# Performance work log

Measured on AMD Instinct MI355X. Metric: run time of the kernel, lower is better.

Reference implementation:

```python
import jax, jax.numpy as jnp
import numpy as np

D = 128
SCALE = 1.0 / np.sqrt(D)  # scalar_value


def setup_inputs() -> dict:
    key = jax.random.key(0)
    k1, k2, k3 = jax.random.split(key, 3)
    B, N, S = 2, 16, 2048
    q = jax.random.normal(k1, (B, N, S, D), dtype=jnp.float32)
    k = jax.random.normal(k2, (B, N, S, D), dtype=jnp.float32)
    v = jax.random.normal(k3, (B, N, S, D), dtype=jnp.float32)
    return {"q": q, "k": k, "v": v}


def reference(q, k, v):
    # BNSD layout. scores = scale * Q K^T, causal mask, softmax with
    # explicit max/sum tracking (golden for NPU fusion attention).
    s1, s2 = q.shape[2], k.shape[2]
    scores = jnp.einsum('bnsd,bntd->bnst', q, k) * SCALE
    # generate_attn_mask: causal (lower-triangular kept), masked -> -inf
    causal = jnp.triu(jnp.ones((s1, s2), dtype=bool), k=1)
    scores = jnp.where(causal, -jnp.inf, scores)
    softmax_max = jnp.max(scores, axis=-1, keepdims=True)          # [B,N,S,1]
    exp_scores = jnp.exp(scores - softmax_max)
    softmax_sum = jnp.sum(exp_scores, axis=-1, keepdims=True)      # [B,N,S,1]
    softmax_res = exp_scores / softmax_sum
    out = jnp.einsum('bnst,bntd->bnsd', softmax_res, v)
    # NPU golden repeats stats x8 along last dim
    return (out,
            jnp.tile(softmax_max, (1, 1, 1, 8)),
            jnp.tile(softmax_sum, (1, 1, 1, 8)))
```

## Files before the change

### kernel.cpp

```cpp
#include <hip/hip_runtime.h>
#include <math.h>
#include <stdint.h>

#define D_DIM 128
#define SEQ 2048
#define NHEADS 32
#define BC 64
#define SCALE 0.08838834764831843f

typedef short bf16x8 __attribute__((ext_vector_type(8)));
typedef float f32x4 __attribute__((ext_vector_type(4)));

union Frag { uint32_t u[4]; bf16x8 v; unsigned short s[8]; };
union Pack8 { unsigned short s[8]; uint4 q; };

__device__ __forceinline__ uint32_t fbits(float x) { return __builtin_bit_cast(uint32_t, x); }
__device__ __forceinline__ float bbits(uint32_t u) { return __builtin_bit_cast(float, u); }
__device__ __forceinline__ unsigned short bf16_rne(float x) {
    uint32_t u = fbits(x);
    u += 0x7FFFu + ((u >> 16) & 1u);
    return (unsigned short)(u >> 16);
}
__device__ __forceinline__ void split2(float a, float b, uint32_t& hp, uint32_t& lp) {
    uint32_t ua = fbits(a) & 0xFFFF0000u, ub = fbits(b) & 0xFFFF0000u;
    float la = a - bbits(ua), lb = b - bbits(ub);
    hp = (ua >> 16) | ub;
    lp = (fbits(la) >> 16) | (fbits(lb) & 0xFFFF0000u);
}

__global__ __launch_bounds__(512, 2) void fa_fused(
    const float* __restrict__ q, const float* __restrict__ k,
    const float* __restrict__ v, float* __restrict__ out)
{
    __shared__ __align__(16) unsigned short Khs[64 * 128];
    __shared__ __align__(16) unsigned short Kls[64 * 128];
    __shared__ __align__(16) unsigned short Vhs[128 * 64];
    __shared__ __align__(16) unsigned short Pbs[128 * 64];

    const int x = blockIdx.x;
    const int it = 15 - (x >> 5);
    const int h = x & 31;

    const int t    = (int)threadIdx.x;
    const int wb   = t >> 6;
    const int lane = t & 63;
    const int ln   = lane & 15;
    const int qd   = lane >> 4;

    const float* qh = q + (size_t)h * SEQ * D_DIM;
    const float* kh = k + (size_t)h * SEQ * D_DIM;
    const float* vh = v + (size_t)h * SEQ * D_DIM;
    float* out_o = out;
    float* out_m = out + (size_t)NHEADS * SEQ * D_DIM;
    float* out_l = out_m + (size_t)NHEADS * SEQ * 8;

    const int qrow0 = it * 128 + wb * 16;

    const int krow0 = t >> 5;
    const int kd4   = t & 31;

    Frag Qh[4], Ql[4];
    {
        const float* qp = qh + (size_t)(qrow0 + ln) * D_DIM;
        #pragma unroll
        for (int kc = 0; kc < 4; ++kc) {
            const int kb = kc * 32 + qd * 8;
            float e[8];
            *(float4*)(e)     = *(const float4*)(qp + kb);
            *(float4*)(e + 4) = *(const float4*)(qp + kb + 4);
            #pragma unroll
            for (int j = 0; j < 8; ++j) e[j] *= SCALE;
            #pragma unroll
            for (int j = 0; j < 4; ++j)
                split2(e[2 * j], e[2 * j + 1], Qh[kc].u[j], Ql[kc].u[j]);
        }
    }

    float4 kreg[4];
    #pragma unroll
    for (int itr = 0; itr < 4; ++itr)
        kreg[itr] = *(const float4*)(kh + (size_t)(itr * 16 + krow0) * D_DIM + kd4 * 4);

    f32x4 accO[8];
    float m_r[4], l_r[4];
    #pragma unroll
    for (int nd = 0; nd < 8; ++nd) accO[nd] = (f32x4){0.f, 0.f, 0.f, 0.f};
    #pragma unroll
    for (int r = 0; r < 4; ++r) { m_r[r] = -INFINITY; l_r[r] = 0.f; }

    const int jt_end = 2 * it + 1;
    for (int jt = 0; jt <= jt_end; ++jt) {
        const int c0 = jt * BC;

        __syncthreads();

        float vreg[2][8];
        #pragma unroll
        for (int uu = 0; uu < 2; ++uu) {
            const int ug = wb * 2 + uu;
            const int cc = ug >> 1;
            const int d  = (ug & 1) * 64 + lane;
            #pragma unroll
            for (int j = 0; j < 8; ++j)
                vreg[uu][j] = vh[(size_t)(c0 + cc * 8 + j) * D_DIM + d];
        }
        #pragma unroll
        for (int itr = 0; itr < 4; ++itr) {
            const int row = itr * 16 + krow0;
            uint32_t hp0, lp0, hp1, lp1;
            split2(kreg[itr].x, kreg[itr].y, hp0, lp0);
            split2(kreg[itr].z, kreg[itr].w, hp1, lp1);
            const int off = row * 128 + (((kd4 >> 1) ^ (row & 7)) * 8) + (kd4 & 1) * 4;
            *(uint2*)(Khs + off) = make_uint2(hp0, hp1);
            *(uint2*)(Kls + off) = make_uint2(lp0, lp1);
        }
        #pragma unroll
        for (int uu = 0; uu < 2; ++uu) {
            const int ug = wb * 2 + uu;
            const int cc = ug >> 1;
            const int d  = (ug & 1) * 64 + lane;
            Pack8 p8;
            #pragma unroll
            for (int j = 0; j < 8; ++j) p8.s[j] = bf16_rne(vreg[uu][j]);
            *(uint4*)(Vhs + d * 64 + ((cc ^ (d & 7)) * 8)) = p8.q;
        }

        __syncthreads();

        if (jt < jt_end) {
            const float* kp2 = kh + (size_t)(c0 + BC) * D_DIM;
            #pragma unroll
            for (int itr = 0; itr < 4; ++itr)
                kreg[itr] = *(const float4*)(kp2 + (size_t)(itr * 16 + krow0) * D_DIM + kd4 * 4);
        }

        if (c0 <= qrow0 + 15) {
            f32x4 accS[4];
            #pragma unroll
            for (int nt = 0; nt < 4; ++nt) accS[nt] = (f32x4){0.f, 0.f, 0.f, 0.f};
            #pragma unroll
            for (int kc = 0; kc < 4; ++kc) {
                #pragma unroll
                for (int nt = 0; nt < 4; ++nt) {
                    int n = nt * 16 + ln;
                    int off = n * 128 + (((kc * 4 + qd) ^ (n & 7)) * 8);
                    Frag Bh, Bl;
                    Bh.v = *(const bf16x8*)(Khs + off);
                    Bl.v = *(const bf16x8*)(Kls + off);
                    f32x4 c = accS[nt];
                    c = __builtin_amdgcn_mfma_f32_16x16x32_bf16(Qh[kc].v, Bh.v, c, 0, 0, 0);
                    c = __builtin_amdgcn_mfma_f32_16x16x32_bf16(Qh[kc].v, Bl.v, c, 0, 0, 0);
                    c = __builtin_amdgcn_mfma_f32_16x16x32_bf16(Ql[kc].v, Bh.v, c, 0, 0, 0);
                    accS[nt] = c;
                }
            }
            const bool needMask = (c0 + 63 > qrow0);
            #pragma unroll
            for (int r = 0; r < 4; ++r) {
                const int rowg = qrow0 + qd * 4 + r;
                float sv[4], mx = -INFINITY;
                #pragma unroll
                for (int nt = 0; nt < 4; ++nt) {
                    float s = accS[nt][r];
                    if (needMask && (c0 + nt * 16 + ln > rowg)) s = -INFINITY;
                    sv[nt] = s; mx = fmaxf(mx, s);
                }
                #pragma unroll
                for (int off = 1; off < 16; off <<= 1) mx = fmaxf(mx, __shfl_xor(mx, off));
                const float mnew = fmaxf(m_r[r], mx);
                const float alpha = __expf(m_r[r] - mnew);
                float p[4];
                #pragma unroll
                for (int nt = 0; nt < 4; ++nt) p[nt] = __expf(sv[nt] - mnew);
                m_r[r] = mnew;
                l_r[r] = l_r[r] * alpha + ((p[0] + p[1]) + (p[2] + p[3]));
                #pragma unroll
                for (int nd = 0; nd < 8; ++nd) accO[nd][r] *= alpha;
                const int R = wb * 16 + qd * 4 + r;
                #pragma unroll
                for (int nt = 0; nt < 4; ++nt) {
                    int c = nt * 16 + ln;
                    Pbs[R * 64 + (((c >> 3) ^ (R & 7)) * 8) + (c & 7)] = bf16_rne(p[nt]);
                }
            }
            #pragma unroll
            for (int kc2 = 0; kc2 < 2; ++kc2) {
                Frag Pf;
                const int R = wb * 16 + ln;
                Pf.v = *(const bf16x8*)(Pbs + R * 64 + (((kc2 * 4 + qd) ^ (R & 7)) * 8));
                #pragma unroll
                for (int nd = 0; nd < 8; ++nd) {
                    int dcol = nd * 16 + ln;
                    int voff = dcol * 64 + (((kc2 * 4 + qd) ^ (dcol & 7)) * 8);
                    Frag Vh2;
                    Vh2.v = *(const bf16x8*)(Vhs + voff);
                    accO[nd] = __builtin_amdgcn_mfma_f32_16x16x32_bf16(Pf.v, Vh2.v, accO[nd], 0, 0, 0);
                }
            }
        }
    }

    #pragma unroll
    for (int r = 0; r < 4; ++r) {
        #pragma unroll
        for (int off = 1; off < 16; off <<= 1) l_r[r] += __shfl_xor(l_r[r], off);
    }
    #pragma unroll
    for (int r = 0; r < 4; ++r) {
        const int rowg = qrow0 + qd * 4 + r;
        const float invl = 1.0f / l_r[r];
        float* op = out_o + (size_t)h * SEQ * D_DIM + (size_t)rowg * D_DIM;
        #pragma unroll
        for (int nd = 0; nd < 8; ++nd) op[nd * 16 + ln] = accO[nd][r] * invl;
        if (ln < 8) {
            size_t sb = ((size_t)h * SEQ + rowg) * 8 + ln;
            out_m[sb] = m_r[r];
            out_l[sb] = l_r[r];
        }
    }
}

extern "C" void kernel_launch(void* const* d_in, const int* in_sizes, int n_in,
                              void* d_out, int out_size, void* d_ws, size_t ws_size,
                              hipStream_t stream) {
    const float* q = (const float*)d_in[0];
    const float* k = (const float*)d_in[1];
    const float* v = (const float*)d_in[2];
    float* out = (float*)d_out;
    (void)d_ws; (void)ws_size;

    fa_fused<<<dim3(512), dim3(512), 0, stream>>>(q, k, v, out);
}
```

Before: 244.6 us.

## Prefetch V tiles into registers and skip rescale when row max unchanged

```diff
diff --git a/kernel.cpp b/kernel.cpp
--- a/kernel.cpp
+++ b/kernel.cpp
@@ -58,6 +58,8 @@
 
     const int krow0 = t >> 5;
     const int kd4   = t & 31;
+    const int vcc   = wb;
+    const int vd0   = lane;
 
     Frag Qh[4], Ql[4];
     {
@@ -77,9 +79,35 @@
     }
 
     float4 kreg[4];
+    float  vraw[2][8];
+    uint2  khi[4], klo[4];
+    uint4  vcv[2];
+
     #pragma unroll
     for (int itr = 0; itr < 4; ++itr)
         kreg[itr] = *(const float4*)(kh + (size_t)(itr * 16 + krow0) * D_DIM + kd4 * 4);
+    #pragma unroll
+    for (int uu = 0; uu < 2; ++uu) {
+        const int d = uu * 64 + vd0;
+        #pragma unroll
+        for (int j = 0; j < 8; ++j)
+            vraw[uu][j] = vh[(size_t)(vcc * 8 + j) * D_DIM + d];
+    }
+    #pragma unroll
+    for (int itr = 0; itr < 4; ++itr) {
+        uint32_t hp0, lp0, hp1, lp1;
+        split2(kreg[itr].x, kreg[itr].y, hp0, lp0);
+        split2(kreg[itr].z, kreg[itr].w, hp1, lp1);
+        khi[itr] = make_uint2(hp0, hp1);
+        klo[itr] = make_uint2(lp0, lp1);
+    }
+    #pragma unroll
+    for (int uu = 0; uu < 2; ++uu) {
+        Pack8 p8;
+        #pragma unroll
+        for (int j = 0; j < 8; ++j) p8.s[j] = bf16_rne(vraw[uu][j]);
+        vcv[uu] = p8.q;
+    }
 
     f32x4 accO[8];
     float m_r[4], l_r[4];
@@ -94,44 +122,34 @@
 
         __syncthreads();
 
-        float vreg[2][8];
-        #pragma unroll
-        for (int uu = 0; uu < 2; ++uu) {
-            const int ug = wb * 2 + uu;
-            const int cc = ug >> 1;
-            const int d  = (ug & 1) * 64 + lane;
-            #pragma unroll
-            for (int j = 0; j < 8; ++j)
-                vreg[uu][j] = vh[(size_t)(c0 + cc * 8 + j) * D_DIM + d];
-        }
         #pragma unroll
         for (int itr = 0; itr < 4; ++itr) {
             const int row = itr * 16 + krow0;
-            uint32_t hp0, lp0, hp1, lp1;
-            split2(kreg[itr].x, kreg[itr].y, hp0, lp0);
-            split2(kreg[itr].z, kreg[itr].w, hp1, lp1);
             const int off = row * 128 + (((kd4 >> 1) ^ (row & 7)) * 8) + (kd4 & 1) * 4;
-            *(uint2*)(Khs + off) = make_uint2(hp0, hp1);
-            *(uint2*)(Kls + off) = make_uint2(lp0, lp1);
+            *(uint2*)(Khs + off) = khi[itr];
+            *(uint2*)(Kls + off) = klo[itr];
         }
         #pragma unroll
         for (int uu = 0; uu < 2; ++uu) {
-            const int ug = wb * 2 + uu;
-            const int cc = ug >> 1;
-            const int d  = (ug & 1) * 64 + lane;
-            Pack8 p8;
-            #pragma unroll
-            for (int j = 0; j < 8; ++j) p8.s[j] = bf16_rne(vreg[uu][j]);
-            *(uint4*)(Vhs + d * 64 + ((cc ^ (d & 7)) * 8)) = p8.q;
+            const int d = uu * 64 + vd0;
+            *(uint4*)(Vhs + d * 64 + ((vcc ^ (d & 7)) * 8)) = vcv[uu];
         }
 
         __syncthreads();
 
         if (jt < jt_end) {
-            const float* kp2 = kh + (size_t)(c0 + BC) * D_DIM;
+            const int c0n = c0 + BC;
+            const float* kp2 = kh + (size_t)c0n * D_DIM;
             #pragma unroll
             for (int itr = 0; itr < 4; ++itr)
                 kreg[itr] = *(const float4*)(kp2 + (size_t)(itr * 16 + krow0) * D_DIM + kd4 * 4);
+            #pragma unroll
+            for (int uu = 0; uu < 2; ++uu) {
+                const int d = uu * 64 + vd0;
+                #pragma unroll
+                for (int j = 0; j < 8; ++j)
+                    vraw[uu][j] = vh[(size_t)(c0n + vcc * 8 + j) * D_DIM + d];
+            }
         }
 
         if (c0 <= qrow0 + 15) {
@@ -155,27 +173,44 @@
                 }
             }
             const bool needMask = (c0 + 63 > qrow0);
+            float mxr[4];
             #pragma unroll
             for (int r = 0; r < 4; ++r) {
                 const int rowg = qrow0 + qd * 4 + r;
-                float sv[4], mx = -INFINITY;
+                float mx = -INFINITY;
                 #pragma unroll
                 for (int nt = 0; nt < 4; ++nt) {
                     float s = accS[nt][r];
                     if (needMask && (c0 + nt * 16 + ln > rowg)) s = -INFINITY;
-                    sv[nt] = s; mx = fmaxf(mx, s);
-                }
-                #pragma unroll
-                for (int off = 1; off < 16; off <<= 1) mx = fmaxf(mx, __shfl_xor(mx, off));
-                const float mnew = fmaxf(m_r[r], mx);
-                const float alpha = __expf(m_r[r] - mnew);
+                    accS[nt][r] = s;
+                    mx = fmaxf(mx, s);
+                }
+                mxr[r] = mx;
+            }
+            #pragma unroll
+            for (int r = 0; r < 4; ++r) {
+                #pragma unroll
+                for (int off = 1; off < 16; off <<= 1) mxr[r] = fmaxf(mxr[r], __shfl_xor(mxr[r], off));
+            }
+            const bool grow = (mxr[0] > m_r[0]) | (mxr[1] > m_r[1]) |
+                              (mxr[2] > m_r[2]) | (mxr[3] > m_r[3]);
+            if (__any(grow)) {
+                #pragma unroll
+                for (int r = 0; r < 4; ++r) {
+                    const float mnew = fmaxf(m_r[r], mxr[r]);
+                    const float alpha = __expf(m_r[r] - mnew);
+                    m_r[r] = mnew;
+                    l_r[r] *= alpha;
+                    #pragma unroll
+                    for (int nd = 0; nd < 8; ++nd) accO[nd][r] *= alpha;
+                }
+            }
+            #pragma unroll
+            for (int r = 0; r < 4; ++r) {
                 float p[4];
                 #pragma unroll
-                for (int nt = 0; nt < 4; ++nt) p[nt] = __expf(sv[nt] - mnew);
-                m_r[r] = mnew;
-                l_r[r] = l_r[r] * alpha + ((p[0] + p[1]) + (p[2] + p[3]));
-                #pragma unroll
-                for (int nd = 0; nd < 8; ++nd) accO[nd][r] *= alpha;
+                for (int nt = 0; nt < 4; ++nt) p[nt] = __expf(accS[nt][r] - m_r[r]);
+                l_r[r] += (p[0] + p[1]) + (p[2] + p[3]);
                 const int R = wb * 16 + qd * 4 + r;
                 #pragma unroll
                 for (int nt = 0; nt < 4; ++nt) {
@@ -196,6 +231,24 @@
                     Vh2.v = *(const bf16x8*)(Vhs + voff);
                     accO[nd] = __builtin_amdgcn_mfma_f32_16x16x32_bf16(Pf.v, Vh2.v, accO[nd], 0, 0, 0);
                 }
+            }
+        }
+
+        if (jt < jt_end) {
+            #pragma unroll
+            for (int itr = 0; itr < 4; ++itr) {
+                uint32_t hp0, lp0, hp1, lp1;
+                split2(kreg[itr].x, kreg[itr].y, hp0, lp0);
+                split2(kreg[itr].z, kreg[itr].w, hp1, lp1);
+                khi[itr] = make_uint2(hp0, hp1);
+                klo[itr] = make_uint2(lp0, lp1);
+            }
+            #pragma unroll
+            for (int uu = 0; uu < 2; ++uu) {
+                Pack8 p8;
+                #pragma unroll
+                for (int j = 0; j < 8; ++j) p8.s[j] = bf16_rne(vraw[uu][j]);
+                vcv[uu] = p8.q;
             }
         }
     }
```

Result: faster. 236.1 us (-3.5%).
